# Kernel tuning notes

Hardware: AMD Instinct MI355X
Metric: run time of the kernel (lower is better)

Reference implementation:

```python
import jax, jax.numpy as jnp
import numpy as np

# dims
B, T, C, D, H, NH, HD, INTER, L = 4, 1024, 256, 256, 512, 8, 64, 2048, 4
CF, CB, BASE = 0, 128, 10000.0  # context_forward, context_backward, rope theta


def _rope_tables():
    inv = 1.0 / (BASE ** (jnp.arange(0, HD, 2, dtype=jnp.float32) / HD))
    t = jnp.arange(T, dtype=jnp.float32)
    f = jnp.einsum('i,j->ij', t, inv)          # [T, HD/2]
    emb = jnp.concatenate([f, f], axis=-1)      # [T, HD]
    return jnp.cos(emb), jnp.sin(emb)


def _rotate_half(x):
    x1, x2 = jnp.split(x, 2, axis=-1)
    return jnp.concatenate([-x2, x1], axis=-1)


def _ln(x, g, b):
    m = x.mean(-1, keepdims=True)
    v = ((x - m) ** 2).mean(-1, keepdims=True)
    return (x - m) / jnp.sqrt(v + 1e-5) * g + b


def _band_mask():
    # create_context_mask(CF, CB, T): allow j in [i-CB, i+CF]
    i = jnp.arange(T)[:, None]
    j = jnp.arange(T)[None, :]
    return (j <= i + CF) & (j >= i - CB)  # [T, T] bool


def setup_inputs() -> dict:
    key = jax.random.key(0)
    ks = jax.random.split(key, 16)
    w = lambda k, shp: (0.02 * jax.random.normal(k, shp)).astype(jnp.float32)
    return {
        'spikes': jax.random.normal(ks[0], (B, T, C), dtype=jnp.float32),
        'spikes_mask': jnp.ones((B, T), dtype=jnp.int32),
        'spikes_timestamp': jnp.tile(jnp.arange(T, dtype=jnp.int32), (B, 1)),
        'embed_w': w(ks[1], (C, D)), 'embed_b': jnp.zeros((D,), jnp.float32),
        'proj_w': w(ks[2], (D, H)), 'proj_b': jnp.zeros((H,), jnp.float32),
        'ln1_g': jnp.ones((L, H), jnp.float32), 'ln1_b': jnp.zeros((L, H), jnp.float32),
        'Wq': w(ks[3], (L, H, H)), 'bq': jnp.zeros((L, H), jnp.float32),
        'Wk': w(ks[4], (L, H, H)), 'bk': jnp.zeros((L, H), jnp.float32),
        'Wv': w(ks[5], (L, H, H)), 'bv': jnp.zeros((L, H), jnp.float32),
        'Wo': w(ks[6], (L, H, H)), 'bo': jnp.zeros((L, H), jnp.float32),
        'ln2_g': jnp.ones((L, H), jnp.float32), 'ln2_b': jnp.zeros((L, H), jnp.float32),
        'up_w': w(ks[7], (L, H, INTER)), 'up_b': jnp.zeros((L, INTER), jnp.float32),
        'down_w': w(ks[8], (L, INTER, H)), 'down_b': jnp.zeros((L, H), jnp.float32),
    }


def reference(spikes, spikes_mask, spikes_timestamp, embed_w, embed_b, proj_w, proj_b,
              ln1_g, ln1_b, Wq, bq, Wk, bk, Wv, bv, Wo, bo, ln2_g, ln2_b,
              up_w, up_b, down_w, down_b):
    cos, sin = _rope_tables()
    mask = _band_mask()[None, None] & (spikes_mask[:, None, None, :] > 0)  # [B,1,T,T]
    cs = cos[spikes_timestamp][:, None]  # [B,1,T,HD]
    sn = sin[spikes_timestamp][:, None]
    neg = jnp.finfo(jnp.float32).min

    # NeuralEmbeddingLayer (no stack/pos/tokens): Linear -> gelu -> Linear
    x = jax.nn.gelu(spikes @ embed_w + embed_b, approximate=False) @ proj_w + proj_b

    for l in range(L):
        h = _ln(x, ln1_g[l], ln1_b[l])
        q = (h @ Wq[l] + bq[l]).reshape(B, T, NH, HD).transpose(0, 2, 1, 3)
        k = (h @ Wk[l] + bk[l]).reshape(B, T, NH, HD).transpose(0, 2, 1, 3)
        v = (h @ Wv[l] + bv[l]).reshape(B, T, NH, HD).transpose(0, 2, 1, 3)
        q = q * cs + _rotate_half(q) * sn
        k = k * cs + _rotate_half(k) * sn
        s = jnp.einsum('bhqd,bhkd->bhqk', q, k) / np.float32(np.sqrt(HD))
        s = jnp.where(mask, s, neg)
        p = jax.nn.softmax(s, axis=-1)
        o = jnp.einsum('bhqk,bhkd->bhqd', p, v).transpose(0, 2, 1, 3).reshape(B, T, H)
        x = x + o @ Wo[l] + bo[l]
        h = _ln(x, ln2_g[l], ln2_b[l])
        x = x + jax.nn.gelu(h @ up_w[l] + up_b[l], approximate=False) @ down_w[l] + down_b[l]
    return x
```

## Files before the change

### kernel.cpp

```cpp
#include <hip/hip_runtime.h>
#include <math.h>

#define B_ 4
#define T_ 1024
#define C_ 256
#define D_ 256
#define H_ 512
#define NH_ 8
#define HD_ 64
#define INTER_ 2048
#define L_ 4
#define CB_ 128

typedef short bf16x8 __attribute__((ext_vector_type(8)));
typedef float f32x4 __attribute__((ext_vector_type(4)));

__device__ __forceinline__ float gelu_exact(float x) {
    return 0.5f * x * (1.0f + erff(x * 0.70710678118654752f));
}

__device__ __forceinline__ unsigned short f2bf(float f) {
    unsigned u = __float_as_uint(f);
    u += 0x7fffu + ((u >> 16) & 1u);
    return (unsigned short)(u >> 16);
}
__device__ __forceinline__ float bf2f(unsigned short h) {
    return __uint_as_float((unsigned)h << 16);
}

template<int ACT, int RES, int OBF, int SPLIT>
__global__ __launch_bounds__(256) void mm64_k(
    const unsigned short* __restrict__ A, const unsigned short* __restrict__ BT,
    const float* __restrict__ b0, const float* __restrict__ b1,
    const float* __restrict__ b2,
    const float* res,
    void* o0, void* o1, void* o2,
    const int M, const int N, const int K)
{
    __shared__ unsigned short As[64 * 64];
    __shared__ unsigned short Bs[64 * 64];

    const int tid  = threadIdx.x;
    const int lane = tid & 63;
    const int w    = tid >> 6;
    const int m0   = blockIdx.y * 64;
    const int n0   = blockIdx.x * 64;
    const int wm   = (w >> 1) * 32;
    const int wn   = (w & 1) * 32;
    const int l16  = lane & 15;
    const int g16  = lane >> 4;

    f32x4 acc[2][2] = {};

    const unsigned short* Abase = A  + (size_t)m0 * K;
    const unsigned short* Bbase = BT + (size_t)n0 * K;

    const int c0 = (w << 6) + lane;
    const int c1 = c0 + 256;
    const int r0c = c0 >> 3, g0c = c0 & 7, gk0 = g0c ^ (r0c & 7);
    const int r1c = c1 >> 3, g1c = c1 & 7, gk1 = g1c ^ (r1c & 7);

    for (int k0 = 0; k0 < K; k0 += 64) {
        __syncthreads();
        __builtin_amdgcn_global_load_lds(
            (const __attribute__((address_space(1))) unsigned*)(Abase + (size_t)r0c * K + k0 + gk0 * 8),
            (__attribute__((address_space(3))) unsigned*)(As + (size_t)(w << 6) * 8), 16, 0, 0);
        __builtin_amdgcn_global_load_lds(
            (const __attribute__((address_space(1))) unsigned*)(Abase + (size_t)r1c * K + k0 + gk1 * 8),
            (__attribute__((address_space(3))) unsigned*)(As + (size_t)(256 + (w << 6)) * 8), 16, 0, 0);
        __builtin_amdgcn_global_load_lds(
            (const __attribute__((address_space(1))) unsigned*)(Bbase + (size_t)r0c * K + k0 + gk0 * 8),
            (__attribute__((address_space(3))) unsigned*)(Bs + (size_t)(w << 6) * 8), 16, 0, 0);
        __builtin_amdgcn_global_load_lds(
            (const __attribute__((address_space(1))) unsigned*)(Bbase + (size_t)r1c * K + k0 + gk1 * 8),
            (__attribute__((address_space(3))) unsigned*)(Bs + (size_t)(256 + (w << 6)) * 8), 16, 0, 0);
        __syncthreads();

#pragma unroll
        for (int kk = 0; kk < 2; ++kk) {
            const int kf = kk * 4 + g16;
            const int sw = (kf ^ (l16 & 7)) * 8;
            bf16x8 a[2], b[2];
#pragma unroll
            for (int t = 0; t < 2; ++t)
                a[t] = *(const bf16x8*)&As[(wm + t * 16 + l16) * 64 + sw];
#pragma unroll
            for (int t = 0; t < 2; ++t)
                b[t] = *(const bf16x8*)&Bs[(wn + t * 16 + l16) * 64 + sw];
#pragma unroll
            for (int i = 0; i < 2; ++i)
#pragma unroll
                for (int j = 0; j < 2; ++j)
                    acc[i][j] = __builtin_amdgcn_mfma_f32_16x16x32_bf16(a[i], b[j], acc[i][j], 0, 0, 0);
        }
    }

    if (OBF || SPLIT) {
        __syncthreads();
        unsigned short* Eb = ((w < 2) ? As : Bs) + (w & 1) * 1024;
        const int row16 = lane >> 2;
        const int cg    = lane & 3;

        const int gnb   = n0 + wn;
        const int which = SPLIT ? (gnb >> 9) : 0;
        const int lnb   = SPLIT ? (gnb & 511) : gnb;
        const int ldo   = SPLIT ? 512 : N;
        unsigned short* oo = SPLIT
            ? ((which == 0) ? (unsigned short*)o0 : (which == 1) ? (unsigned short*)o1 : (unsigned short*)o2)
            : (unsigned short*)o0;
        const float* bb = SPLIT ? ((which == 0) ? b0 : (which == 1) ? b1 : b2) : b0;
        const float scale = (SPLIT && which == 0) ? 0.125f : 1.0f;

#pragma unroll
        for (int i = 0; i < 2; ++i) {
#pragma unroll
            for (int j = 0; j < 2; ++j) {
                const float bv = bb[lnb + j * 16 + l16];
#pragma unroll
                for (int r = 0; r < 4; ++r) {
                    float cv = acc[i][j][r] + bv;
                    if (ACT) cv = gelu_exact(cv);
                    if (SPLIT) cv *= scale;
                    Eb[(g16 * 4 + r) * 40 + j * 16 + l16] = f2bf(cv);
                }
            }
            const int grow0 = m0 + wm + i * 16 + row16;
#pragma unroll
            for (int s = 0; s < 2; ++s) {
                ushort4 t4 = *(const ushort4*)&Eb[row16 * 40 + s * 16 + cg * 4];
                *(ushort4*)&oo[(size_t)grow0 * ldo + lnb + s * 16 + cg * 4] = t4;
            }
        }
        return;
    }

#pragma unroll
    for (int i = 0; i < 2; ++i) {
        const int gmb = m0 + wm + i * 16 + g16 * 4;
#pragma unroll
        for (int j = 0; j < 2; ++j) {
            const int gn = n0 + wn + j * 16 + l16;
            const float bv = b0[gn];
#pragma unroll
            for (int r = 0; r < 4; ++r) {
                float cv = acc[i][j][r] + bv;
                if (ACT) cv = gelu_exact(cv);
                if (RES) cv += res[(size_t)(gmb + r) * 512 + gn];
                ((float*)o0)[(size_t)(gmb + r) * N + gn] = cv;
            }
        }
    }
}

__global__ __launch_bounds__(256) void prep_k(
    const float* __restrict__ spikes,
    const float* __restrict__ embed_w, const float* __restrict__ proj_w,
    const float* __restrict__ Wq, const float* __restrict__ Wk,
    const float* __restrict__ Wv, const float* __restrict__ Wo,
    const float* __restrict__ up_w, const float* __restrict__ down_w,
    unsigned short* __restrict__ spbf,
    unsigned short* __restrict__ embT, unsigned short* __restrict__ projT,
    unsigned short* __restrict__ qkvT, unsigned short* __restrict__ woT,
    unsigned short* __restrict__ upT, unsigned short* __restrict__ downT)
{
    const int idx = blockIdx.x;
    const int tid = threadIdx.x;

    if (idx >= 3120) {
        const int base = (idx - 3120) * 4096 + tid * 16;
#pragma unroll
        for (int s = 0; s < 4; ++s) {
            float4 v = *(const float4*)&spikes[base + s * 4];
            ushort4 o = {f2bf(v.x), f2bf(v.y), f2bf(v.z), f2bf(v.w)};
            *(ushort4*)&spbf[base + s * 4] = o;
        }
        return;
    }

    const float* src; unsigned short* dst; int R, Cc, t;
    if (idx < 16)      { src = embed_w; dst = embT;  R = C_; Cc = D_; t = idx; }
    else if (idx < 48) { src = proj_w;  dst = projT; R = D_; Cc = H_; t = idx - 16; }
    else if (idx < 816) {
        const int j = idx - 48;
        const int wsel = j >> 8;
        const int l = (j & 255) >> 6;
        t = j & 63;
        src = ((wsel == 0) ? Wq : (wsel == 1) ? Wk : Wv) + (size_t)l * H_ * H_;
        dst = qkvT + (size_t)l * 3 * H_ * H_ + (size_t)wsel * H_ * H_;
        R = H_; Cc = H_;
    } else if (idx < 1072) {
        const int j = idx - 816; const int l = j >> 6; t = j & 63;
        src = Wo + (size_t)l * H_ * H_; dst = woT + (size_t)l * H_ * H_;
        R = H_; Cc = H_;
    } else if (idx < 2096) {
        const int j = idx - 1072; const int l = j >> 8; t = j & 255;
        src = up_w + (size_t)l * H_ * INTER_; dst = upT + (size_t)l * INTER_ * H_;
        R = H_; Cc = INTER_;
    } else {
        const int j = idx - 2096; const int l = j >> 8; t = j & 255;
        src = down_w + (size_t)l * INTER_ * H_; dst = downT + (size_t)l * H_ * INTER_;
        R = INTER_; Cc = H_;
    }
    const int ntx = Cc >> 6;
    const int c0 = (t % ntx) * 64, r0 = (t / ntx) * 64;

    __shared__ float tile[64][65];
    const int tr = tid >> 4, tc = (tid & 15) * 4;
#pragma unroll
    for (int i = 0; i < 4; ++i) {
        float4 v = *(const float4*)&src[(size_t)(r0 + tr + i * 16) * Cc + c0 + tc];
        tile[tr + i * 16][tc + 0] = v.x;
        tile[tr + i * 16][tc + 1] = v.y;
        tile[tr + i * 16][tc + 2] = v.z;
        tile[tr + i * 16][tc + 3] = v.w;
    }
    __syncthreads();
#pragma unroll
    for (int i = 0; i < 4; ++i) {
        const int n = tr + i * 16;
        ushort4 o;
        o.x = f2bf(tile[tc + 0][n]);
        o.y = f2bf(tile[tc + 1][n]);
        o.z = f2bf(tile[tc + 2][n]);
        o.w = f2bf(tile[tc + 3][n]);
        *(ushort4*)&dst[(size_t)(c0 + n) * R + r0 + tc] = o;
    }
}

__global__ __launch_bounds__(256) void ln_k(
    const float* __restrict__ x, const float* __restrict__ g,
    const float* __restrict__ b, unsigned short* __restrict__ out)
{
    const int row = blockIdx.x;
    const int tid = threadIdx.x;
    const float* xr = x + (size_t)row * H_;

    float v0 = xr[tid];
    float v1 = xr[tid + 256];

    float s = v0 + v1;
#pragma unroll
    for (int off = 32; off; off >>= 1) s += __shfl_xor(s, off);

    __shared__ float red[4];
    const int wave = tid >> 6;
    if ((tid & 63) == 0) red[wave] = s;
    __syncthreads();
    const float mean = (red[0] + red[1] + red[2] + red[3]) * (1.0f / (float)H_);

    const float d0 = v0 - mean, d1 = v1 - mean;
    float q = d0 * d0 + d1 * d1;
#pragma unroll
    for (int off = 32; off; off >>= 1) q += __shfl_xor(q, off);
    __syncthreads();
    if ((tid & 63) == 0) red[wave] = q;
    __syncthreads();
    const float var = (red[0] + red[1] + red[2] + red[3]) * (1.0f / (float)H_);
    const float rstd = rsqrtf(var + 1e-5f);

    out[(size_t)row * H_ + tid]       = f2bf(d0 * rstd * g[tid] + b[tid]);
    out[(size_t)row * H_ + tid + 256] = f2bf(d1 * rstd * g[tid + 256] + b[tid + 256]);
}

#define AWIN 192
#define AKS 72
#define AVS 200

__global__ __launch_bounds__(256) void attn_k(
    const unsigned short* __restrict__ q, const unsigned short* __restrict__ k,
    const unsigned short* __restrict__ v, const int* __restrict__ smask,
    const int* __restrict__ ts, unsigned short* __restrict__ o)
{
    __shared__ unsigned short Qs[64 * AKS];
    __shared__ unsigned short Ks[AWIN * AKS];
    __shared__ unsigned short Vt[64 * AVS];
    unsigned short* const Pb = Ks;

    const int blk = blockIdx.x;
    const int qt = blk & 15;
    const int h  = (blk >> 4) & 7;
    const int b  = blk >> 7;
    const int tid  = threadIdx.x;
    const int lane = tid & 63;
    const int w    = tid >> 6;
    const int l16  = lane & 15;
    const int g16  = lane >> 4;

    const int qlo = qt * 64;
    const int klo = (qlo >= CB_) ? (qlo - CB_) : 0;
    const int tb  = b * 1024;

    {
        const unsigned short* gq = q + ((size_t)(tb + qlo)) * 512 + h * 64;
        for (int c = tid; c < 64 * 8; c += 256) {
            const int row = c >> 3, c4 = (c & 7) * 4;
            ushort4 lo = *(const ushort4*)&gq[(size_t)row * 512 + c4];
            ushort4 hi = *(const ushort4*)&gq[(size_t)row * 512 + c4 + 32];
            const float tstamp = (float)ts[tb + qlo + row];
            ushort4 olo, ohi;
#pragma unroll
            for (int j2 = 0; j2 < 4; ++j2) {
                const float freq = __expf(-0.2878231366242558f * (float)(c4 + j2));
                const float ang = tstamp * freq;
                const float cc = __cosf(ang), ss = __sinf(ang);
                const float v1 = bf2f(((const unsigned short*)&lo)[j2]);
                const float v2 = bf2f(((const unsigned short*)&hi)[j2]);
                ((unsigned short*)&olo)[j2] = f2bf(v1 * cc - v2 * ss);
                ((unsigned short*)&ohi)[j2] = f2bf(v2 * cc + v1 * ss);
            }
            *(ushort4*)&Qs[row * AKS + c4]      = olo;
            *(ushort4*)&Qs[row * AKS + c4 + 32] = ohi;
        }
    }
    {
        const unsigned short* gk = k + ((size_t)(tb + klo)) * 512 + h * 64;
        for (int c = tid; c < AWIN * 8; c += 256) {
            const int row = c >> 3, c4 = (c & 7) * 4;
            ushort4 lo = *(const ushort4*)&gk[(size_t)row * 512 + c4];
            ushort4 hi = *(const ushort4*)&gk[(size_t)row * 512 + c4 + 32];
            const float tstamp = (float)ts[tb + klo + row];
            ushort4 olo, ohi;
#pragma unroll
            for (int j2 = 0; j2 < 4; ++j2) {
                const float freq = __expf(-0.2878231366242558f * (float)(c4 + j2));
                const float ang = tstamp * freq;
                const float cc = __cosf(ang), ss = __sinf(ang);
                const float v1 = bf2f(((const unsigned short*)&lo)[j2]);
                const float v2 = bf2f(((const unsigned short*)&hi)[j2]);
                ((unsigned short*)&olo)[j2] = f2bf(v1 * cc - v2 * ss);
                ((unsigned short*)&ohi)[j2] = f2bf(v2 * cc + v1 * ss);
            }
            *(ushort4*)&Ks[row * AKS + c4]      = olo;
            *(ushort4*)&Ks[row * AKS + c4 + 32] = ohi;
        }
    }
    {
        const unsigned short* gv = v + ((size_t)(tb + klo)) * 512 + h * 64;
        for (int c = tid; c < AWIN * 16; c += 256) {
            const int row = c >> 4, c4 = (c & 15) * 4;
            ushort4 vv = *(const ushort4*)&gv[(size_t)row * 512 + c4];
            Vt[(c4 + 0) * AVS + row] = vv.x;
            Vt[(c4 + 1) * AVS + row] = vv.y;
            Vt[(c4 + 2) * AVS + row] = vv.z;
            Vt[(c4 + 3) * AVS + row] = vv.w;
        }
    }
    __syncthreads();

    f32x4 accs[12];
    {
        const bf16x8 a0 = *(const bf16x8*)&Qs[(w * 16 + l16) * AKS + g16 * 8];
        const bf16x8 a1 = *(const bf16x8*)&Qs[(w * 16 + l16) * AKS + 32 + g16 * 8];
#pragma unroll
        for (int t = 0; t < 12; ++t) {
            const bf16x8 b0 = *(const bf16x8*)&Ks[(t * 16 + l16) * AKS + g16 * 8];
            const bf16x8 b1 = *(const bf16x8*)&Ks[(t * 16 + l16) * AKS + 32 + g16 * 8];
            f32x4 c = {};
            c = __builtin_amdgcn_mfma_f32_16x16x32_bf16(a0, b0, c, 0, 0, 0);
            c = __builtin_amdgcn_mfma_f32_16x16x32_bf16(a1, b1, c, 0, 0, 0);
            accs[t] = c;
        }
    }

    bool mk[12];
    int  jj[12];
#pragma unroll
    for (int t = 0; t < 12; ++t) {
        jj[t] = klo + t * 16 + l16;
        mk[t] = smask[tb + jj[t]] > 0;
    }

    float rs[4];
#pragma unroll
    for (int r = 0; r < 4; ++r) {
        const int i = qlo + 16 * w + g16 * 4 + r;
        float mx = -1e30f;
#pragma unroll
        for (int t = 0; t < 12; ++t) {
            const bool val = mk[t] && (jj[t] >= i - CB_) && (jj[t] <= i);
            mx = fmaxf(mx, val ? accs[t][r] : -1e30f);
        }
        mx = fmaxf(mx, __shfl_xor(mx, 1));
        mx = fmaxf(mx, __shfl_xor(mx, 2));
        mx = fmaxf(mx, __shfl_xor(mx, 4));
        mx = fmaxf(mx, __shfl_xor(mx, 8));
        float sum = 0.0f;
#pragma unroll
        for (int t = 0; t < 12; ++t) {
            const bool val = mk[t] && (jj[t] >= i - CB_) && (jj[t] <= i);
            const float p = val ? __expf(accs[t][r] - mx) : 0.0f;
            accs[t][r] = p;
            sum += p;
        }
        sum += __shfl_xor(sum, 1);
        sum += __shfl_xor(sum, 2);
        sum += __shfl_xor(sum, 4);
        sum += __shfl_xor(sum, 8);
        rs[r] = 1.0f / sum;
    }

    __syncthreads();

#pragma unroll
    for (int t = 0; t < 12; ++t)
#pragma unroll
        for (int r = 0; r < 4; ++r)
            Pb[(16 * w + g16 * 4 + r) * AVS + t * 16 + l16] = f2bf(accs[t][r]);

    f32x4 acco[4];
#pragma unroll
    for (int nt = 0; nt < 4; ++nt) {
        f32x4 c = {};
#pragma unroll
        for (int ks = 0; ks < 6; ++ks) {
            const bf16x8 a = *(const bf16x8*)&Pb[(16 * w + l16) * AVS + ks * 32 + g16 * 8];
            const bf16x8 bb = *(const bf16x8*)&Vt[(nt * 16 + l16) * AVS + ks * 32 + g16 * 8];
            c = __builtin_amdgcn_mfma_f32_16x16x32_bf16(a, bb, c, 0, 0, 0);
        }
        acco[nt] = c;
    }

    __syncthreads();
#pragma unroll
    for (int nt = 0; nt < 4; ++nt)
#pragma unroll
        for (int r = 0; r < 4; ++r)
            Pb[(16 * w + g16 * 4 + r) * AVS + nt * 16 + l16] = f2bf(acco[nt][r] * rs[r]);

    const int row16 = lane >> 2, cg = lane & 3;
    const int grow = tb + qlo + 16 * w + row16;
#pragma unroll
    for (int s = 0; s < 4; ++s) {
        ushort4 t4 = *(const ushort4*)&Pb[(16 * w + row16) * AVS + s * 16 + cg * 4];
        *(ushort4*)&o[(size_t)grow * 512 + h * 64 + s * 16 + cg * 4] = t4;
    }
}

extern "C" void kernel_launch(void* const* d_in, const int* in_sizes, int n_in,
                              void* d_out, int out_size, void* d_ws, size_t ws_size,
                              hipStream_t stream)
{
    const float* spikes  = (const float*)d_in[0];
    const int*   smask   = (const int*)d_in[1];
    const int*   ts      = (const int*)d_in[2];
    const float* embed_w = (const float*)d_in[3];
    const float* embed_b = (const float*)d_in[4];
    const float* proj_w  = (const float*)d_in[5];
    const float* proj_b  = (const float*)d_in[6];
    const float* ln1_g   = (const float*)d_in[7];
    const float* ln1_b   = (const float*)d_in[8];
    const float* Wq      = (const float*)d_in[9];
    const float* bq      = (const float*)d_in[10];
    const float* Wk      = (const float*)d_in[11];
    const float* bk      = (const float*)d_in[12];
    const float* Wv      = (const float*)d_in[13];
    const float* bv      = (const float*)d_in[14];
    const float* Wo      = (const float*)d_in[15];
    const float* bo      = (const float*)d_in[16];
    const float* ln2_g   = (const float*)d_in[17];
    const float* ln2_b   = (const float*)d_in[18];
    const float* up_w    = (const float*)d_in[19];
    const float* up_b    = (const float*)d_in[20];
    const float* down_w  = (const float*)d_in[21];
    const float* down_b  = (const float*)d_in[22];

    const int M = B_ * T_;

    char* p = (char*)d_ws;
    float* x = (float*)p;                       p += (size_t)M * H_ * 4;
    unsigned short* qb  = (unsigned short*)p;   p += (size_t)M * H_ * 2;
    unsigned short* kb  = (unsigned short*)p;   p += (size_t)M * H_ * 2;
    unsigned short* vb  = (unsigned short*)p;   p += (size_t)M * H_ * 2;
    unsigned short* hbf = (unsigned short*)p;   p += (size_t)M * H_ * 2;
    unsigned short* obf = (unsigned short*)p;   p += (size_t)M * H_ * 2;
    unsigned short* ibf = (unsigned short*)p;   p += (size_t)M * INTER_ * 2;
    unsigned short* tbf = (unsigned short*)p;   p += (size_t)M * D_ * 2;
    unsigned short* spbf  = (unsigned short*)p; p += (size_t)M * C_ * 2;
    unsigned short* embT  = (unsigned short*)p; p += (size_t)D_ * C_ * 2;
    unsigned short* projT = (unsigned short*)p; p += (size_t)H_ * D_ * 2;
    unsigned short* qkvT  = (unsigned short*)p; p += (size_t)L_ * 3 * H_ * H_ * 2;
    unsigned short* woT   = (unsigned short*)p; p += (size_t)L_ * H_ * H_ * 2;
    unsigned short* upT   = (unsigned short*)p; p += (size_t)L_ * INTER_ * H_ * 2;
    unsigned short* downT = (unsigned short*)p; p += (size_t)L_ * H_ * INTER_ * 2;

    prep_k<<<3376, 256, 0, stream>>>(
        spikes, embed_w, proj_w, Wq, Wk, Wv, Wo, up_w, down_w,
        spbf, embT, projT, qkvT, woT, upT, downT);

    mm64_k<1, 0, 1, 0><<<dim3(D_ / 64, M / 64), 256, 0, stream>>>(
        spbf, embT, embed_b, nullptr, nullptr, nullptr,
        tbf, nullptr, nullptr, M, D_, C_);
    mm64_k<0, 0, 0, 0><<<dim3(H_ / 64, M / 64), 256, 0, stream>>>(
        tbf, projT, proj_b, nullptr, nullptr, nullptr,
        x, nullptr, nullptr, M, H_, D_);

    for (int l = 0; l < L_; ++l) {
        const unsigned short* qkvT_l = qkvT + (size_t)l * 3 * H_ * H_;
        const unsigned short* woT_l  = woT  + (size_t)l * H_ * H_;
        const unsigned short* upT_l  = upT  + (size_t)l * INTER_ * H_;
        const unsigned short* dnT_l  = downT + (size_t)l * H_ * INTER_;

        ln_k<<<M, 256, 0, stream>>>(x, ln1_g + l * H_, ln1_b + l * H_, hbf);

        mm64_k<0, 0, 1, 1><<<dim3((3 * H_) / 64, M / 64), 256, 0, stream>>>(
            hbf, qkvT_l, bq + l * H_, bk + l * H_, bv + l * H_, nullptr,
            qb, kb, vb, M, 3 * H_, H_);

        attn_k<<<B_ * NH_ * (T_ / 64), 256, 0, stream>>>(qb, kb, vb, smask, ts, obf);

        mm64_k<0, 1, 0, 0><<<dim3(H_ / 64, M / 64), 256, 0, stream>>>(
            obf, woT_l, bo + l * H_, nullptr, nullptr, x,
            x, nullptr, nullptr, M, H_, H_);

        ln_k<<<M, 256, 0, stream>>>(x, ln2_g + l * H_, ln2_b + l * H_, hbf);

        mm64_k<1, 0, 1, 0><<<dim3(INTER_ / 64, M / 64), 256, 0, stream>>>(
            hbf, upT_l, up_b + l * INTER_, nullptr, nullptr, nullptr,
            ibf, nullptr, nullptr, M, INTER_, H_);

        float* dst = (l == L_ - 1) ? (float*)d_out : x;
        mm64_k<0, 1, 0, 0><<<dim3(H_ / 64, M / 64), 256, 0, stream>>>(
            ibf, dnT_l, down_b + l * H_, nullptr, nullptr, x,
            dst, nullptr, nullptr, M, H_, INTER_);
    }
}
```

Measured before the change: 547.1 us.

## Add 128x64 GEMM tile for QKV and up-proj, plus XCD-aware block swizzle

Adds an mm128_k kernel in which each block computes a 128x64 output tile, with each wave holding 4x2 MFMA accumulators. It is used for the QKV and up-projection GEMMs to raise arithmetic intensity and reduce how often B-tile loads repeat. It also adds a block-index swizzle to all GEMMs so that consecutive tiles map to the same XCD, which should improve L2 locality. In exchange, there are fewer blocks per launch (lower occupancy and parallelism), and the swizzle assumes the workgroup count is divisible by 8.

```diff
diff --git a/kernel.cpp b/kernel.cpp
--- a/kernel.cpp
+++ b/kernel.cpp
@@ -26,6 +26,15 @@
 }
 __device__ __forceinline__ float bf2f(unsigned short h) {
     return __uint_as_float((unsigned)h << 16);
+}
+
+__device__ __forceinline__ void xcd_swz(int& bx, int& by) {
+    const int gx  = gridDim.x;
+    const int nwg = gx * gridDim.y;
+    int bid = blockIdx.y * gx + blockIdx.x;
+    bid = (bid & 7) * (nwg >> 3) + (bid >> 3);
+    bx = bid % gx;
+    by = bid / gx;
 }
 
 template<int ACT, int RES, int OBF, int SPLIT>
@@ -40,11 +49,13 @@
     __shared__ unsigned short As[64 * 64];
     __shared__ unsigned short Bs[64 * 64];
 
+    int bx, by; xcd_swz(bx, by);
+
     const int tid  = threadIdx.x;
     const int lane = tid & 63;
     const int w    = tid >> 6;
-    const int m0   = blockIdx.y * 64;
-    const int n0   = blockIdx.x * 64;
+    const int m0   = by * 64;
+    const int n0   = bx * 64;
     const int wm   = (w >> 1) * 32;
     const int wn   = (w & 1) * 32;
     const int l16  = lane & 15;
@@ -136,6 +147,132 @@
 
 #pragma unroll
     for (int i = 0; i < 2; ++i) {
+        const int gmb = m0 + wm + i * 16 + g16 * 4;
+#pragma unroll
+        for (int j = 0; j < 2; ++j) {
+            const int gn = n0 + wn + j * 16 + l16;
+            const float bv = b0[gn];
+#pragma unroll
+            for (int r = 0; r < 4; ++r) {
+                float cv = acc[i][j][r] + bv;
+                if (ACT) cv = gelu_exact(cv);
+                if (RES) cv += res[(size_t)(gmb + r) * 512 + gn];
+                ((float*)o0)[(size_t)(gmb + r) * N + gn] = cv;
+            }
+        }
+    }
+}
+
+template<int ACT, int RES, int OBF, int SPLIT>
+__global__ __launch_bounds__(256) void mm128_k(
+    const unsigned short* __restrict__ A, const unsigned short* __restrict__ BT,
+    const float* __restrict__ b0, const float* __restrict__ b1,
+    const float* __restrict__ b2,
+    const float* res,
+    void* o0, void* o1, void* o2,
+    const int M, const int N, const int K)
+{
+    __shared__ unsigned short As[128 * 64];
+    __shared__ unsigned short Bs[64 * 64];
+
+    int bx, by; xcd_swz(bx, by);
+
+    const int tid  = threadIdx.x;
+    const int lane = tid & 63;
+    const int w    = tid >> 6;
+    const int m0   = by * 128;
+    const int n0   = bx * 64;
+    const int wm   = (w >> 1) * 64;
+    const int wn   = (w & 1) * 32;
+    const int l16  = lane & 15;
+    const int g16  = lane >> 4;
+
+    f32x4 acc[4][2] = {};
+
+    const unsigned short* Abase = A  + (size_t)m0 * K;
+    const unsigned short* Bbase = BT + (size_t)n0 * K;
+
+    for (int k0 = 0; k0 < K; k0 += 64) {
+        __syncthreads();
+#pragma unroll
+        for (int it = 0; it < 4; ++it) {
+            const int c = it * 256 + tid;
+            const int rc = c >> 3, gk = (c & 7) ^ (rc & 7);
+            __builtin_amdgcn_global_load_lds(
+                (const __attribute__((address_space(1))) unsigned*)(Abase + (size_t)rc * K + k0 + gk * 8),
+                (__attribute__((address_space(3))) unsigned*)(As + (size_t)(it * 256 + (w << 6)) * 8), 16, 0, 0);
+        }
+#pragma unroll
+        for (int it = 0; it < 2; ++it) {
+            const int c = it * 256 + tid;
+            const int rc = c >> 3, gk = (c & 7) ^ (rc & 7);
+            __builtin_amdgcn_global_load_lds(
+                (const __attribute__((address_space(1))) unsigned*)(Bbase + (size_t)rc * K + k0 + gk * 8),
+                (__attribute__((address_space(3))) unsigned*)(Bs + (size_t)(it * 256 + (w << 6)) * 8), 16, 0, 0);
+        }
+        __syncthreads();
+
+#pragma unroll
+        for (int kk = 0; kk < 2; ++kk) {
+            const int kf = kk * 4 + g16;
+            const int sw = (kf ^ (l16 & 7)) * 8;
+            bf16x8 a[4], b[2];
+#pragma unroll
+            for (int t = 0; t < 4; ++t)
+                a[t] = *(const bf16x8*)&As[(wm + t * 16 + l16) * 64 + sw];
+#pragma unroll
+            for (int t = 0; t < 2; ++t)
+                b[t] = *(const bf16x8*)&Bs[(wn + t * 16 + l16) * 64 + sw];
+#pragma unroll
+            for (int i = 0; i < 4; ++i)
+#pragma unroll
+                for (int j = 0; j < 2; ++j)
+                    acc[i][j] = __builtin_amdgcn_mfma_f32_16x16x32_bf16(a[i], b[j], acc[i][j], 0, 0, 0);
+        }
+    }
+
+    if (OBF || SPLIT) {
+        __syncthreads();
+        constexpr int EST = 40;
+        unsigned short* Eb = As + w * (16 * EST);
+        const int erow = lane >> 3;
+        const int ecol = (lane & 7) * 4;
+
+        const int gnb   = n0 + wn;
+        const int which = SPLIT ? (gnb >> 9) : 0;
+        const int lnb   = SPLIT ? (gnb & 511) : gnb;
+        const int ldo   = SPLIT ? 512 : N;
+        unsigned short* oo = SPLIT
+            ? ((which == 0) ? (unsigned short*)o0 : (which == 1) ? (unsigned short*)o1 : (unsigned short*)o2)
+            : (unsigned short*)o0;
+        const float* bb = SPLIT ? ((which == 0) ? b0 : (which == 1) ? b1 : b2) : b0;
+        const float scale = (SPLIT && which == 0) ? 0.125f : 1.0f;
+
+#pragma unroll
+        for (int i = 0; i < 4; ++i) {
+#pragma unroll
+            for (int j = 0; j < 2; ++j) {
+                const float bv = bb[lnb + j * 16 + l16];
+#pragma unroll
+                for (int r = 0; r < 4; ++r) {
+                    float cv = acc[i][j][r] + bv;
+                    if (ACT) cv = gelu_exact(cv);
+                    if (SPLIT) cv *= scale;
+                    Eb[(g16 * 4 + r) * EST + j * 16 + l16] = f2bf(cv);
+                }
+            }
+            const int grow0 = m0 + wm + i * 16;
+#pragma unroll
+            for (int s = 0; s < 2; ++s) {
+                ushort4 t4 = *(const ushort4*)&Eb[(s * 8 + erow) * EST + ecol];
+                *(ushort4*)&oo[(size_t)(grow0 + s * 8 + erow) * ldo + lnb + ecol] = t4;
+            }
+        }
+        return;
+    }
+
+#pragma unroll
+    for (int i = 0; i < 4; ++i) {
         const int gmb = m0 + wm + i * 16 + g16 * 4;
 #pragma unroll
         for (int j = 0; j < 2; ++j) {
@@ -502,7 +639,7 @@
 
         ln_k<<<M, 256, 0, stream>>>(x, ln1_g + l * H_, ln1_b + l * H_, hbf);
 
-        mm64_k<0, 0, 1, 1><<<dim3((3 * H_) / 64, M / 64), 256, 0, stream>>>(
+        mm128_k<0, 0, 1, 1><<<dim3((3 * H_) / 64, M / 128), 256, 0, stream>>>(
             hbf, qkvT_l, bq + l * H_, bk + l * H_, bv + l * H_, nullptr,
             qb, kb, vb, M, 3 * H_, H_);
 
@@ -514,7 +651,7 @@
 
         ln_k<<<M, 256, 0, stream>>>(x, ln2_g + l * H_, ln2_b + l * H_, hbf);
 
-        mm64_k<1, 0, 1, 0><<<dim3(INTER_ / 64, M / 64), 256, 0, stream>>>(
+        mm128_k<1, 0, 1, 0><<<dim3(INTER_ / 64, M / 128), 256, 0, stream>>>(
             hbf, upT_l, up_b + l * INTER_, nullptr, nullptr, nullptr,
             ibf, nullptr, nullptr, M, INTER_, H_);
 
```

New measurement: 516.1 us. -5.7%, faster.
